# Kernel tuning notes

Measured on AMD Instinct MI355X. Metric: run time of the kernel, lower is better.

Reference implementation:

```python
import jax, jax.numpy as jnp
import numpy as np
from jax import lax

B = 2
IMG = 640.0
MIN_LEVEL, MAX_LEVEL = 3, 7
NUM_CLASSES = 91          # includes background (index 0)
MAX_TOTAL = 100
IOU_THR = 0.3
SCORE_THR = 0.05
PRE_NMS = 5000
BBOX_CLIP = float(np.log(1000.0 / 16.0))  # standard box-transform clip


def _level_anchors(level):
    """RetinaNet-style anchors for one pyramid level, [H*W*9, 4] in (y1,x1,y2,x2)."""
    stride = 2 ** level
    feat = int(IMG) // stride
    cy = (np.arange(feat, dtype=np.float32) + 0.5) * stride
    cx = (np.arange(feat, dtype=np.float32) + 0.5) * stride
    cy, cx = np.meshgrid(cy, cx, indexing='ij')
    base = 4.0 * stride
    anchors = []
    for octave in (2 ** 0.0, 2 ** (1.0 / 3.0), 2 ** (2.0 / 3.0)):
        for ar in (0.5, 1.0, 2.0):
            h = base * octave * np.sqrt(ar)
            w = base * octave / np.sqrt(ar)
            anchors.append(np.stack([cy - h / 2, cx - w / 2, cy + h / 2, cx + w / 2], -1))
    a = np.stack(anchors, -2).reshape(-1, 4)
    return a.astype(np.float32)


def setup_inputs():
    key = jax.random.key(0)
    inp = {}
    for level in range(MIN_LEVEL, MAX_LEVEL + 1):
        anc = _level_anchors(level)
        n = anc.shape[0]
        key, kb, kc = jax.random.split(key, 3)
        inp[f'box_outputs_{level}'] = 0.2 * jax.random.normal(kb, (B, n, 4), jnp.float32)
        inp[f'class_outputs_{level}'] = jax.random.normal(kc, (B, n, NUM_CLASSES), jnp.float32) - 2.0
        inp[f'anchor_boxes_{level}'] = jnp.broadcast_to(jnp.asarray(anc)[None], (B, n, 4))
    inp['image_shape'] = jnp.full((B, 2), IMG, jnp.float32)
    return inp


def _decode_boxes(enc, anchors):
    # faithful to box_utils.decode_boxes (with the +1/-1 pixel convention)
    dy, dx = enc[..., 0], enc[..., 1]
    dh = jnp.minimum(enc[..., 2], BBOX_CLIP)
    dw = jnp.minimum(enc[..., 3], BBOX_CLIP)
    ah = anchors[..., 2] - anchors[..., 0] + 1.0
    aw = anchors[..., 3] - anchors[..., 1] + 1.0
    ayc = anchors[..., 0] + 0.5 * ah
    axc = anchors[..., 1] + 0.5 * aw
    yc = dy * ah + ayc
    xc = dx * aw + axc
    h = jnp.exp(dh) * ah
    w = jnp.exp(dw) * aw
    ymin = yc - 0.5 * h
    xmin = xc - 0.5 * w
    return jnp.stack([ymin, xmin, ymin + h - 1.0, xmin + w - 1.0], axis=-1)


def _clip_boxes(boxes, image_shape):
    h = image_shape[:, 0:1]
    w = image_shape[:, 1:2]
    max_len = jnp.stack([h, w, h, w], axis=-1)  # [B,1,4]
    return jnp.clip(boxes, 0.0, max_len)


def _greedy_nms(scores, boxes):
    """Sorted greedy NMS over one (batch, class) lane.
    scores: [K] sorted descending (filtered entries are -1), boxes: [K,4].
    Returns top MAX_TOTAL selected (score, box) in descending score order,
    padded with score=-1 / zero boxes (matches sorted_non_max_suppression_padded).
    """
    areas = (boxes[:, 2] - boxes[:, 0]) * (boxes[:, 3] - boxes[:, 1])

    def step(active, _):
        masked = jnp.where(active, scores, -jnp.inf)
        i = jnp.argmax(masked)
        s = masked[i]
        valid = s > -1.0
        b = boxes[i]
        yy1 = jnp.maximum(b[0], boxes[:, 0])
        xx1 = jnp.maximum(b[1], boxes[:, 1])
        yy2 = jnp.minimum(b[2], boxes[:, 2])
        xx2 = jnp.minimum(b[3], boxes[:, 3])
        inter = jnp.maximum(yy2 - yy1, 0.0) * jnp.maximum(xx2 - xx1, 0.0)
        iou = inter / ((b[2] - b[0]) * (b[3] - b[1]) + areas - inter + 1e-8)
        active = active & (iou <= IOU_THR)
        active = active.at[i].set(False)
        out_s = jnp.where(valid, s, -1.0)
        out_b = jnp.where(valid, b, jnp.zeros_like(b))
        return active, (out_s, out_b)

    _, (sel_s, sel_b) = lax.scan(step, jnp.ones(scores.shape[0], bool), None, length=MAX_TOTAL)
    return sel_s, sel_b


def reference(box_outputs_3, box_outputs_4, box_outputs_5, box_outputs_6, box_outputs_7,
              class_outputs_3, class_outputs_4, class_outputs_5, class_outputs_6, class_outputs_7,
              anchor_boxes_3, anchor_boxes_4, anchor_boxes_5, anchor_boxes_6, anchor_boxes_7,
              image_shape):
    box_list = [box_outputs_3, box_outputs_4, box_outputs_5, box_outputs_6, box_outputs_7]
    cls_list = [class_outputs_3, class_outputs_4, class_outputs_5, class_outputs_6, class_outputs_7]
    anc_list = [anchor_boxes_3, anchor_boxes_4, anchor_boxes_5, anchor_boxes_6, anchor_boxes_7]

    boxes, scores = [], []
    for bo, co, an in zip(box_list, cls_list, anc_list):
        scores.append(jax.nn.sigmoid(co)[..., 1:])            # drop background class 0
        boxes.append(_clip_boxes(_decode_boxes(bo, an), image_shape))
    boxes = jnp.concatenate(boxes, axis=1)                     # [B,N,4] class-agnostic
    scores = jnp.concatenate(scores, axis=1)                   # [B,N,C]

    scores_t = jnp.transpose(scores, (0, 2, 1))                # [B,C,N]
    k = min(scores_t.shape[-1], PRE_NMS)
    top_s, idx = lax.top_k(scores_t, k)                        # [B,C,K]
    top_b = jax.vmap(lambda b, i: b[i])(boxes, idx)            # [B,C,K,4]

    # filter_boxes_by_scores: score -> -1, boxes -> 0 below threshold
    mask = top_s >= SCORE_THR
    top_s = jnp.where(mask, top_s, -1.0)
    top_b = top_b * mask[..., None].astype(top_b.dtype)

    sel_s, sel_b = jax.vmap(jax.vmap(_greedy_nms))(top_s, top_b)  # [B,C,T], [B,C,T,4]
    Bsz, C, T = sel_s.shape
    classes = jnp.broadcast_to(jnp.arange(C, dtype=jnp.int32)[None, :, None], (Bsz, C, T))

    flat_s = sel_s.reshape(Bsz, C * T)
    flat_b = sel_b.reshape(Bsz, C * T, 4)
    flat_c = classes.reshape(Bsz, C * T)

    final_s, fidx = lax.top_k(flat_s, MAX_TOTAL)
    final_b = jnp.take_along_axis(flat_b, fidx[..., None], axis=1)
    final_c = jnp.take_along_axis(flat_c, fidx, axis=1) + 1    # nmsed_classes += 1
    valid = jnp.sum((final_s > -1.0).astype(jnp.int32), axis=1)
    return final_b, final_s, final_c, valid
```

## Files before the change

### kernel.cpp

```cpp
#include <hip/hip_runtime.h>
#include <hip/hip_bf16.h>

typedef unsigned long long u64;
typedef unsigned int u32;

#define A_TOTAL 76725
#define NCLS 90
#define KTOP 5000u
#define MAXT 100
#define KTHR 0x3D4CCCCDu
#define TCAP 2048u
#define NSEL 384u

__device__ __forceinline__ u64 pack_key(u32 k, u32 i) {
  return ((u64)k << 32) | (u64)(0xFFFFFFFFu - i);
}

__device__ __forceinline__ int dig05(u64 k) {
  float s = __uint_as_float((u32)(k >> 32));
  int d = (int)((s - 0.5f) * 8175.0f);
  return min(max(d, 0), 4095);
}

__device__ __forceinline__ void cut4096w(const u32* hh, u32 need, int wl,
                                         u32& B, u32& incl, u32& above, u32& total) {
  int lo = wl << 6;
  u32 s = 0;
  #pragma unroll
  for (int j = 0; j < 64; ++j) s += hh[lo + j];
  u32 suf = s;
  #pragma unroll
  for (int off = 1; off < 64; off <<= 1) {
    u32 v = __shfl_down(suf, off, 64);
    if (wl < 64 - off) suf += v;
  }
  total = __shfl(suf, 0, 64);
  if (total < need) { B = 0; incl = total; above = 0; return; }
  u32 sufnext = suf - s;
  bool cross = (suf >= need) && (sufnext < need);
  u64 bal = __ballot(cross);
  int gl = (int)__ffsll((unsigned long long)bal) - 1;
  int glo = gl << 6;
  u32 aboveG = __shfl(sufnext, gl, 64);
  u32 hb = hh[glo + wl];
  u32 sufb = hb;
  #pragma unroll
  for (int off = 1; off < 64; off <<= 1) {
    u32 v = __shfl_down(sufb, off, 64);
    if (wl < 64 - off) sufb += v;
  }
  bool c2 = (aboveG + sufb >= need) && (aboveG + sufb - hb < need);
  u64 bal2 = __ballot(c2);
  int jB = (int)__ffsll((unsigned long long)bal2) - 1;
  B = (u32)(glo + jB);
  incl = aboveG + __shfl(sufb, jB, 64);
  above = incl - __shfl(hb, jB, 64);
}

__device__ __forceinline__ void bitonic_desc(u64* a, u32 n, int tid, int nth) {
  u32 P = 2; while (P < n) P <<= 1;
  for (u32 i = tid; i < P; i += nth) if (i >= n) a[i] = 0ULL;
  __syncthreads();
  for (u32 kk = 2; kk <= P; kk <<= 1) {
    for (u32 jj = kk >> 1; jj; jj >>= 1) {
      for (u32 i = tid; i < P; i += nth) {
        u32 ixj = i ^ jj;
        if (ixj > i) {
          u64 x = a[i], y = a[ixj];
          bool up = ((i & kk) == 0);
          if (up ? (x < y) : (x > y)) { a[i] = y; a[ixj] = x; }
        }
      }
      __syncthreads();
    }
  }
}

__device__ __forceinline__ int lazy_scan_g(const u64* key_s, const float4* boxes4, size_t bbase,
                                           int C, float4* wbox, float* outS, float* outB,
                                           int w, int wl, int* endCur) {
  int cur = 0;
  while (w < MAXT && cur < C) {
    int p = cur + wl;
    bool alive = (p < C);
    u64 kk = alive ? key_s[p] : 0ull;
    float4 mybox = make_float4(0.f, 0.f, 0.f, 0.f);
    if (alive) {
      u32 idx = 0xFFFFFFFFu - (u32)(kk & 0xFFFFFFFFull);
      mybox = boxes4[bbase + idx];
    }
    float myarea = alive ? (mybox.z - mybox.x) * (mybox.w - mybox.y) : 0.f;
    for (int j = 0; j < w; ++j) {
      if (alive) {
        float4 pb = wbox[j];
        float yy1 = fmaxf(pb.x, mybox.x), xx1 = fmaxf(pb.y, mybox.y);
        float yy2 = fminf(pb.z, mybox.z), xx2 = fminf(pb.w, mybox.w);
        float inter = fmaxf(yy2 - yy1, 0.0f) * fmaxf(xx2 - xx1, 0.0f);
        float pa = (pb.z - pb.x) * (pb.w - pb.y);
        if (inter / (pa + myarea - inter + 1e-8f) > 0.3f) alive = false;
      }
    }
    for (;;) {
      u64 bal = __ballot(alive);
      if (bal == 0ull) break;
      int js = (int)__ffsll((unsigned long long)bal) - 1;
      float4 pb;
      pb.x = __shfl(mybox.x, js, 64);
      pb.y = __shfl(mybox.y, js, 64);
      pb.z = __shfl(mybox.z, js, 64);
      pb.w = __shfl(mybox.w, js, 64);
      u64 wk = __shfl(kk, js, 64);
      if (wl == 0) {
        outS[w] = __uint_as_float((u32)(wk >> 32));
        *(float4*)(outB + w * 4) = pb;
        wbox[w] = pb;
      }
      w++;
      if (w >= MAXT) break;
      if (wl <= js) alive = false;
      else if (alive) {
        float yy1 = fmaxf(pb.x, mybox.x), xx1 = fmaxf(pb.y, mybox.y);
        float yy2 = fminf(pb.z, mybox.z), xx2 = fminf(pb.w, mybox.w);
        float inter = fmaxf(yy2 - yy1, 0.0f) * fmaxf(xx2 - xx1, 0.0f);
        float pa = (pb.z - pb.x) * (pb.w - pb.y);
        if (inter / (pa + myarea - inter + 1e-8f) > 0.3f) alive = false;
      }
    }
    cur += 64;
  }
  *endCur = cur;
  return w;
}

__device__ __forceinline__ void coll_elem(int i, float x, int b, int base,
                                          u64* __restrict__ listT_g, u32* __restrict__ cnt_pad) {
  if (x >= 0.0f) {
    u32 a = (u32)i / 91u;
    u32 c = (u32)i - a * 91u;
    if (c != 0u) {
      float s = 1.0f / (1.0f + expf(-x));
      int lane = b * NCLS + (int)c - 1;
      u32 idx = (u32)base + a;
      u32 p = atomicAdd(&cnt_pad[lane * 64], 1u);
      if (p < TCAP) listT_g[(size_t)lane * TCAP + p] = pack_key(__float_as_uint(s), idx);
    }
  }
}

__global__ __launch_bounds__(256) void front_kernel(
    const float* __restrict__ bx0, const float* __restrict__ bx1, const float* __restrict__ bx2,
    const float* __restrict__ bx3, const float* __restrict__ bx4,
    const float* __restrict__ an0, const float* __restrict__ an1, const float* __restrict__ an2,
    const float* __restrict__ an3, const float* __restrict__ an4,
    const float* __restrict__ c3, const float* __restrict__ c4, const float* __restrict__ c5,
    const float* __restrict__ c6, const float* __restrict__ c7,
    const float* __restrict__ img, float* __restrict__ boxes,
    u64* __restrict__ listT_g, u32* __restrict__ cnt_pad)
{
  int blk = blockIdx.x, tid = threadIdx.x;
  if (blk < 600) {
    int t = blk * 256 + tid;
    if (t >= 2 * A_TOTAL) return;
    int b = t / A_TOTAL, a = t % A_TOTAL;
    const float* bp; const float* ap; int al; int nl;
    if (a < 57600)      { bp = bx0; ap = an0; al = a;          nl = 57600; }
    else if (a < 72000) { bp = bx1; ap = an1; al = a - 57600;  nl = 14400; }
    else if (a < 75600) { bp = bx2; ap = an2; al = a - 72000;  nl = 3600;  }
    else if (a < 76500) { bp = bx3; ap = an3; al = a - 75600;  nl = 900;   }
    else                { bp = bx4; ap = an4; al = a - 76500;  nl = 225;   }
    float4 e  = *(const float4*)(bp + ((size_t)b * nl + al) * 4);
    float4 an = *(const float4*)(ap + ((size_t)b * nl + al) * 4);
    const float CLIP = 4.135166556742356f;
    float ah  = an.z - an.x + 1.0f;
    float aw  = an.w - an.y + 1.0f;
    float ayc = an.x + 0.5f * ah;
    float axc = an.y + 0.5f * aw;
    float dh = fminf(e.z, CLIP), dw = fminf(e.w, CLIP);
    float yc = e.x * ah + ayc;
    float xc = e.y * aw + axc;
    float h  = expf(dh) * ah;
    float w  = expf(dw) * aw;
    float ymin = yc - 0.5f * h;
    float xmin = xc - 0.5f * w;
    float ymax = ymin + h - 1.0f;
    float xmax = xmin + w - 1.0f;
    float H = img[b * 2 + 0], W = img[b * 2 + 1];
    float4 o;
    o.x = fminf(fmaxf(ymin, 0.0f), H);
    o.y = fminf(fmaxf(xmin, 0.0f), W);
    o.z = fminf(fmaxf(ymax, 0.0f), H);
    o.w = fminf(fmaxf(xmax, 0.0f), W);
    *(float4*)(boxes + (size_t)t * 4) = o;
    return;
  }
  int blk2 = blk - 600;
  const float* cls; int n, base, b, loc, J, lvl;
  if (blk2 < 1280)      { lvl = 0; cls = c3; n = 57600; base = 0;     J = 640; int r = blk2;        b = r >= J; loc = b ? r - J : r; }
  else if (blk2 < 1600) { lvl = 1; cls = c4; n = 14400; base = 57600; J = 160; int r = blk2 - 1280; b = r >= J; loc = b ? r - J : r; }
  else if (blk2 < 1680) { lvl = 2; cls = c5; n = 3600;  base = 72000; J = 40;  int r = blk2 - 1600; b = r >= J; loc = b ? r - J : r; }
  else if (blk2 < 1700) { lvl = 3; cls = c6; n = 900;   base = 75600; J = 10;  int r = blk2 - 1680; b = r >= J; loc = b ? r - J : r; }
  else                  { lvl = 4; cls = c7; n = 225;   base = 76500; J = 5;   int r = blk2 - 1700; b = r >= J; loc = b ? r - J : r; }

  if (lvl <= 3) {
    int F4 = n * 91 / 4;
    int chunk = (F4 + J - 1) / J;
    int q0 = loc * chunk;
    int q1 = q0 + chunk; if (q1 > F4) q1 = F4;
    const float4* src4 = (const float4*)(cls + (size_t)b * n * 91);
    for (int q = q0 + tid; q < q1; q += 256) {
      float4 v = src4[q];
      int i0 = q << 2;
      coll_elem(i0,     v.x, b, base, listT_g, cnt_pad);
      coll_elem(i0 + 1, v.y, b, base, listT_g, cnt_pad);
      coll_elem(i0 + 2, v.z, b, base, listT_g, cnt_pad);
      coll_elem(i0 + 3, v.w, b, base, listT_g, cnt_pad);
    }
  } else {
    int F = n * 91;
    int chunk = (F + J - 1) / J;
    int s0 = loc * chunk;
    int s1 = s0 + chunk; if (s1 > F) s1 = F;
    const float* src = cls + (size_t)b * F;
    for (int i = s0 + tid; i < s1; i += 256) coll_elem(i, src[i], b, base, listT_g, cnt_pad);
  }
}

__global__ __launch_bounds__(256) void nms_kernel(
    const float* __restrict__ c3, const float* __restrict__ c4, const float* __restrict__ c5,
    const float* __restrict__ c6, const float* __restrict__ c7,
    const float* __restrict__ boxes, const u64* __restrict__ listT_g,
    const u32* __restrict__ cnt_pad, float* __restrict__ nms_s, float* __restrict__ nms_b)
{
  __shared__ __align__(16) char big[40960];
  __shared__ __align__(16) u64 listE[2048];
  __shared__ u64 key_s[2048];
  __shared__ __align__(16) u32 histL[4096];
  __shared__ float4 wbox[MAXT];
  __shared__ u32 wtot[4];
  __shared__ u32 sh_flag, sh_mid, sh_bigS, sh_cS;
  __shared__ u64 sh_minPrev;
  __shared__ u32 sh_w, sh_done, sh_eidx, sh_Rthr, sh_eSorted, sh_bigF;
  __shared__ u32 sh_B, sh_incl, sh_above, sh_total, sh_cA, sh_cE, sh_B2;

  int tid = threadIdx.x;
  int lane = blockIdx.x;
  int b = lane / NCLS, c = lane % NCLS;
  const float4* boxes4 = (const float4*)boxes;
  size_t bbase = (size_t)b * A_TOTAL;
  const u64 thrpack = ((u64)KTHR) << 32;

  float* outS = nms_s + (size_t)lane * MAXT;
  float* outB = nms_b + (size_t)lane * MAXT * 4;

  u32 cnt = cnt_pad[lane * 64];
  if (tid == 0) { sh_flag = (cnt > TCAP) ? 1u : 0u; sh_mid = 0; sh_bigS = 0; }
  __syncthreads();

  if (!sh_flag) {
    const u64* LT = listT_g + (size_t)lane * TCAP;
    u64 kr[8];
    #pragma unroll
    for (int r = 0; r < 8; ++r) {
      u32 s = (u32)tid + (u32)r * 256u;
      kr[r] = (s < cnt) ? LT[s] : 0ull;
    }

    for (int i = tid; i < 4096; i += 256) histL[i] = 0;
    __syncthreads();
    #pragma unroll
    for (int r = 0; r < 8; ++r) if (kr[r]) atomicAdd(&histL[dig05(kr[r])], 1u);
    __syncthreads();
    if (tid < 64) {
      u32 Bx, ix, ax, tx;
      cut4096w(histL, NSEL, tid, Bx, ix, ax, tx);
      if (tid == 0) { sh_B = Bx; sh_incl = ix; sh_total = tx; sh_cS = 0; }
    }
    __syncthreads();
    u32 B = sh_B, incl = sh_incl, total = sh_total;
    bool selAll = (total < NSEL);
    u32 Csel = selAll ? total : incl;
    if (Csel <= 768u) {
      u64* sel = (u64*)histL;
      #pragma unroll
      for (int r = 0; r < 8; ++r) {
        u64 k = kr[r];
        if (k && (selAll || (u32)dig05(k) >= B)) {
          u32 p = atomicAdd(&sh_cS, 1u);
          if (p < 768u) sel[p] = k;
        }
      }
      __syncthreads();
      u32 Cs = sh_cS; if (Cs > 768u) Cs = 768u;
      for (u32 j = tid; j < Cs; j += 256) {
        u64 kj = sel[j];
        u32 rk = 0;
        for (u32 i2 = 0; i2 < Cs; ++i2) rk += (sel[i2] > kj) ? 1u : 0u;
        key_s[rk] = kj;
      }
      __syncthreads();
      if (tid < 64) {
        int ec;
        int w = lazy_scan_g(key_s, boxes4, bbase, (int)Cs, wbox, outS, outB, 0, tid, &ec);
        if (tid == 0) {
          sh_w = (u32)w;
          if (w < MAXT) { if (selAll) sh_flag = 1; else sh_mid = 1; }
          else if (!selAll && ec > (int)Cs - 64) sh_mid = 1;
        }
      }
    } else {
      if (tid == 0) sh_mid = 1;
    }
    __syncthreads();

    if (sh_mid && !sh_flag) {
      for (int i = tid; i < 4096; i += 256) histL[i] = 0;
      if (tid == 0) sh_bigS = 0;
      __syncthreads();
      #pragma unroll
      for (int r = 0; r < 8; ++r) if (kr[r]) atomicAdd(&histL[dig05(kr[r])], 1u);
      __syncthreads();
      {
        int t0 = tid << 4;
        u32 hloc[16]; u32 ssum = 0;
        #pragma unroll
        for (int j = 0; j < 16; ++j) { hloc[j] = histL[t0 + j]; ssum += hloc[j]; }
        int wl = tid & 63, wid = tid >> 6;
        u32 suf = ssum;
        #pragma unroll
        for (int off = 1; off < 64; off <<= 1) {
          u32 v = __shfl_down(suf, off, 64);
          if (wl < 64 - off) suf += v;
        }
        if (wl == 0) wtot[wid] = suf;
        __syncthreads();
        u32 cross = 0;
        for (int w2 = wid + 1; w2 < 4; ++w2) cross += wtot[w2];
        u32 run = (suf - ssum) + cross;
        #pragma unroll
        for (int j = 15; j >= 0; --j) { u32 b2 = run; run += hloc[j]; histL[t0 + j] = b2; }
      }
      __syncthreads();
      #pragma unroll
      for (int r = 0; r < 8; ++r) {
        u64 k = kr[r];
        if (k) {
          u32 pos = atomicAdd(&histL[dig05(k)], 1u);
          if (pos < TCAP) key_s[pos] = k;
        }
      }
      __syncthreads();
      {
        int t0 = tid << 4;
        for (int j = 0; j < 16; ++j) {
          u32 d = (u32)(t0 + j);
          u32 end = histL[d];
          u32 start = (d == 4095u) ? 0u : histL[d + 1];
          u32 cc = end - start;
          if (cc >= 2u) {
            if (cc <= 48u) {
              for (u32 a2 = start + 1; a2 < end; ++a2) {
                u64 kv = key_s[a2];
                int bi = (int)a2 - 1;
                while (bi >= (int)start && key_s[bi] < kv) { key_s[bi + 1] = key_s[bi]; --bi; }
                key_s[bi + 1] = kv;
              }
            } else sh_bigS = 1;
          }
        }
      }
      __syncthreads();
      if (sh_bigS) bitonic_desc(key_s, cnt, tid, 256);
      if (tid < 64) {
        int ec;
        int w = lazy_scan_g(key_s, boxes4, bbase, (int)cnt, wbox, outS, outB, 0, tid, &ec);
        if (tid == 0) {
          sh_w = (u32)w;
          if (w < MAXT) sh_flag = 1;
        }
      }
    }
  }
  __syncthreads();
  if (!sh_flag) {
    u32 w = sh_w;
    for (u32 p = w + (u32)tid; p < MAXT; p += 256) {
      outS[p] = -1.0f;
      *(float4*)(outB + p * 4) = make_float4(0.f, 0.f, 0.f, 0.f);
    }
    return;
  }

  auto sb_of = [&](int i) -> u32 {
    const float* p; int al, nl;
    if (i < 57600)      { p = c3; al = i;          nl = 57600; }
    else if (i < 72000) { p = c4; al = i - 57600;  nl = 14400; }
    else if (i < 75600) { p = c5; al = i - 72000;  nl = 3600;  }
    else if (i < 76500) { p = c6; al = i - 75600;  nl = 900;   }
    else                { p = c7; al = i - 76500;  nl = 225;   }
    float x = p[((size_t)b * nl + al) * 91 + (c + 1)];
    float s = 1.0f / (1.0f + expf(-x));
    return __float_as_uint(s);
  };

  u64* listA = (u64*)big;
  for (int i = tid; i < 4096; i += 256) histL[i] = 0;
  if (tid == 0) {
    sh_cA = 0; sh_cE = 0; sh_w = 0; sh_done = 0; sh_eidx = 0; sh_eSorted = 0; sh_minPrev = ~0ull;
  }
  __syncthreads();
  for (int i = tid; i < A_TOTAL; i += 256) atomicAdd(&histL[sb_of(i) >> 19], 1u);
  __syncthreads();
  if (tid < 64) {
    u32 Bx, ix, ax, tx;
    cut4096w(histL, KTOP, tid, Bx, ix, ax, tx);
    if (tid == 0) sh_B = Bx;
  }
  __syncthreads();
  u32 B = sh_B;
  for (int i = tid; i < A_TOTAL; i += 256) {
    u32 u = sb_of(i);
    u32 bkt = u >> 19;
    if (bkt > B) {
      u32 p = atomicAdd(&sh_cA, 1u);
      if (p < 5120u) listA[p] = pack_key(u, (u32)i);
    } else if (bkt == B) {
      u32 p = atomicAdd(&sh_cE, 1u);
      if (p < 2048u) listE[p] = pack_key(u, (u32)i);
    }
  }
  __syncthreads();
  u32 g = sh_cA, h = sh_cE;
  if (h > 2048u) {
    for (int i = tid; i < 4096; i += 256) histL[i] = 0;
    if (tid == 0) sh_cE = 0;
    __syncthreads();
    for (int i = tid; i < A_TOTAL; i += 256) {
      u32 u = sb_of(i);
      if ((u >> 19) == B) atomicAdd(&histL[(u >> 7) & 0xFFFu], 1u);
    }
    __syncthreads();
    u32 R1 = KTOP - g;
    if (tid < 64) {
      u32 Bx, ix, ax, tx;
      cut4096w(histL, R1, tid, Bx, ix, ax, tx);
      if (tid == 0) sh_B2 = Bx;
    }
    __syncthreads();
    u32 B2 = sh_B2;
    for (int i = tid; i < A_TOTAL; i += 256) {
      u32 u = sb_of(i);
      if ((u >> 19) == B) {
        u32 sb2 = (u >> 7) & 0xFFFu;
        if (sb2 > B2) {
          u32 p = atomicAdd(&sh_cA, 1u);
          if (p < 5120u) listA[p] = pack_key(u, (u32)i);
        } else if (sb2 == B2) {
          u32 p = atomicAdd(&sh_cE, 1u);
          if (p < 2048u) listE[p] = pack_key(u, (u32)i);
        }
      }
    }
    __syncthreads();
    g = sh_cA; h = sh_cE; if (h > 2048u) h = 2048u;
  }
  if (g > 5120u) g = 5120u;
  u32 R = (g < KTOP) ? (KTOP - g) : 0u; if (R > h) R = h;

  u64 ak[20];
  #pragma unroll
  for (int r = 0; r < 20; ++r) {
    u32 s2 = (u32)tid + (u32)r * 256u;
    u64 kp = (s2 < g) ? listA[s2] : 0ull;
    if (kp < thrpack) kp = 0ull;
    ak[r] = kp;
  }
  __syncthreads();
  u32* cntArr = (u32*)big;

  const float LO0  = 0.04f;
  const float INV0 = 4096.0f / (1.001f - 0.04f);

  for (int seg = 0; seg < 7200; ++seg) {
    __syncthreads();
    if (sh_w >= MAXT || sh_done) break;
    u64 minPrev = sh_minPrev;

    int digLvl = 0;
    u32 A_B0 = 0, A_B1 = 0;
    float lo1 = 0.f, inv1 = 0.f;
    u64 kMask = 0, kPref = 0;
    int m1shift = 32;
    int selMode = -1;
    u32 selB = 0;
    u32 C = 0;
    bool fromE = false;

    for (int lvl = 0; lvl < 8; ++lvl) {
      for (int i = tid; i < 4096; i += 256) histL[i] = 0;
      __syncthreads();
      #pragma unroll
      for (int r = 0; r < 20; ++r) {
        u64 k = ak[r];
        if (!k || k >= minPrev) continue;
        float s = __uint_as_float((u32)(k >> 32));
        if (digLvl >= 1) { int d0 = (int)((s - LO0) * INV0); d0 = min(max(d0, 0), 4095); if ((u32)d0 != A_B0) continue; }
        if (digLvl >= 2) { int d1 = (int)((s - lo1) * inv1); d1 = min(max(d1, 0), 4095); if ((u32)d1 != A_B1) continue; }
        if (digLvl >= 3 && ((k & kMask) != kPref)) continue;
        u32 d;
        if (digLvl == 0)      { int t0 = (int)((s - LO0) * INV0); d = (u32)min(max(t0, 0), 4095); }
        else if (digLvl == 1) { int t1 = (int)((s - lo1) * inv1); d = (u32)min(max(t1, 0), 4095); }
        else                  d = (u32)((k >> m1shift) & 0xFFFull);
        atomicAdd(&histL[d], 1u);
      }
      __syncthreads();
      if (tid < 64) {
        u32 Bx, ix, ax, tx;
        cut4096w(histL, 1024u, tid, Bx, ix, ax, tx);
        if (tid == 0) { sh_B = Bx; sh_incl = ix; sh_above = ax; sh_total = tx; }
      }
      __syncthreads();
      u32 total = sh_total, incl = sh_incl, above = sh_above, Bx = sh_B;
      if (total == 0u)   { fromE = true; break; }
      if (total < 1024u) { selMode = 0; C = total; break; }
      if (incl <= 2048u) { selMode = 1; selB = Bx; C = incl; break; }
      if (above > 0u)    { selMode = 2; selB = Bx; C = above; break; }
      if (digLvl == 0) {
        A_B0 = Bx;
        lo1 = LO0 + (float)Bx / INV0;
        inv1 = INV0 * 4096.0f;
        digLvl = 1;
      } else if (digLvl == 1) {
        A_B1 = Bx;
        digLvl = 2; m1shift = 32;
      } else {
        kPref |= ((u64)Bx << m1shift);
        kMask |= (0xFFFull << m1shift);
        m1shift -= 12;
        digLvl++;
      }
      __syncthreads();
    }

    if (fromE) {
      if (!sh_eSorted) {
        bitonic_desc(listE, h, tid, 256);
        if (tid == 0) {
          u32 lo = 0, hi2 = h;
          while (lo < hi2) { u32 mid = (lo + hi2) >> 1; if (listE[mid] >= thrpack) lo = mid + 1; else hi2 = mid; }
          sh_Rthr = (R < lo) ? R : lo;
          sh_eSorted = 1;
        }
        __syncthreads();
      }
      u32 eidx = sh_eidx;
      u32 take = (sh_Rthr > eidx) ? (sh_Rthr - eidx) : 0u;
      if (take > 2048u) take = 2048u;
      if (take == 0u) { if (tid == 0) sh_done = 1; continue; }
      for (u32 i = tid; i < take; i += 256) key_s[i] = listE[eidx + i];
      C = take;
      if (tid == 0) sh_eidx = eidx + take;
    } else {
      u32 hloc[16];
      {
        int t0 = tid << 4;
        u32 ssum = 0;
        #pragma unroll
        for (int j = 0; j < 16; ++j) { hloc[j] = histL[t0 + j]; ssum += hloc[j]; }
        int wl = tid & 63, wid = tid >> 6;
        u32 suf = ssum;
        #pragma unroll
        for (int off = 1; off < 64; off <<= 1) {
          u32 v = __shfl_down(suf, off, 64);
          if (wl < 64 - off) suf += v;
        }
        if (wl == 0) wtot[wid] = suf;
        __syncthreads();
        u32 cross = 0;
        for (int w2 = wid + 1; w2 < 4; ++w2) cross += wtot[w2];
        u32 run = (suf - ssum) + cross;
        #pragma unroll
        for (int j = 15; j >= 0; --j) { u32 base2 = run; run += hloc[j]; histL[t0 + j] = base2; }
      }
      for (int i = tid; i < 4096; i += 256) cntArr[i] = 0;
      if (tid == 0) sh_bigF = 0;
      __syncthreads();
      #pragma unroll
      for (int r = 0; r < 20; ++r) {
        u64 k = ak[r];
        if (!k || k >= minPrev) continue;
        float s = __uint_as_float((u32)(k >> 32));
        if (digLvl >= 1) { int d0 = (int)((s - LO0) * INV0); d0 = min(max(d0, 0), 4095); if ((u32)d0 != A_B0) continue; }
        if (digLvl >= 2) { int d1 = (int)((s - lo1) * inv1); d1 = min(max(d1, 0), 4095); if ((u32)d1 != A_B1) continue; }
        if (digLvl >= 3 && ((k & kMask) != kPref)) continue;
        u32 d;
        if (digLvl == 0)      { int t0x = (int)((s - LO0) * INV0); d = (u32)min(max(t0x, 0), 4095); }
        else if (digLvl == 1) { int t1x = (int)((s - lo1) * inv1); d = (u32)min(max(t1x, 0), 4095); }
        else                  d = (u32)((k >> m1shift) & 0xFFFull);
        if (selMode == 1)      { if (d < selB) continue; }
        else if (selMode == 2) { if (d <= selB) continue; }
        u32 pos = histL[d] + atomicAdd(&cntArr[d], 1u);
        if (pos < 2048u) key_s[pos] = k;
      }
      __syncthreads();
      {
        int t0 = tid << 4;
        for (int j = 0; j < 16; ++j) {
          u32 bkt = (u32)(t0 + j);
          u32 cc = cntArr[bkt];
          if (cc >= 2u) {
            if (cc <= 48u) {
              u32 basep = histL[bkt];
              for (u32 a2 = 1; a2 < cc; ++a2) {
                u64 kv = key_s[basep + a2];
                int bi = (int)a2 - 1;
                while (bi >= 0 && key_s[basep + bi] < kv) { key_s[basep + bi + 1] = key_s[basep + bi]; --bi; }
                key_s[basep + bi + 1] = kv;
              }
            } else sh_bigF = 1;
          }
        }
      }
      __syncthreads();
      if (sh_bigF) bitonic_desc(key_s, C, tid, 256);
      if (tid == 0) sh_minPrev = key_s[C - 1];
    }
    __syncthreads();

    if (tid < 64) {
      int ec;
      int w = lazy_scan_g(key_s, boxes4, bbase, (int)C, wbox, outS, outB, (int)sh_w, tid, &ec);
      if (tid == 0) sh_w = (u32)w;
    }
  }

  __syncthreads();
  u32 w = sh_w;
  for (u32 p = w + (u32)tid; p < MAXT; p += 256) {
    outS[p] = -1.0f;
    *(float4*)(outB + p * 4) = make_float4(0.f, 0.f, 0.f, 0.f);
  }
}

__global__ __launch_bounds__(256) void merge_kernel(
    const float* __restrict__ nms_s, const float* __restrict__ nms_b,
    float* __restrict__ out_b, float* __restrict__ out_s,
    float* __restrict__ out_c, float* __restrict__ out_v)
{
  __shared__ u64 keys[NCLS * MAXT];
  __shared__ u32 hist[4096];
  __shared__ u64 sel[640];
  __shared__ u32 sh_cnt, sh_valid;
  __shared__ u32 sh_B, sh_incl, sh_above, sh_total;

  int b = blockIdx.x, tid = threadIdx.x;
  const int NTOT = NCLS * MAXT;

  for (int i = tid; i < NTOT; i += 256) {
    float s = nms_s[(size_t)b * NTOT + i];
    u32 u = __float_as_uint(s);
    u = (u & 0x80000000u) ? ~u : (u | 0x80000000u);
    keys[i] = ((u64)u << 32) | (u64)(0xFFFFFFFFu - (u32)i);
  }
  if (tid == 0) { sh_cnt = 0; sh_valid = 0; }

  u64 prefVal = 0;
  u64 T = 0;
  u32 need = MAXT;
  const int shifts[6] = {52, 40, 28, 16, 4, 0};
  const int widths[6] = {12, 12, 12, 12, 12, 4};
  for (int lvl = 0; lvl < 6; ++lvl) {
    int s = shifts[lvl], w = widths[lvl];
    for (int i = tid; i < 4096; i += 256) hist[i] = 0;
    __syncthreads();
    u32 dmask = (1u << w) - 1u;
    for (int i = tid; i < NTOT; i += 256) {
      u64 k = keys[i];
      if (lvl > 0 && (k >> (s + w)) != (prefVal >> (s + w))) continue;
      atomicAdd(&hist[(u32)((k >> s) & dmask)], 1u);
    }
    __syncthreads();
    if (tid < 64) {
      u32 Bx, ix, ax, tx;
      cut4096w(hist, need, tid, Bx, ix, ax, tx);
      if (tid == 0) { sh_B = Bx; sh_incl = ix; sh_above = ax; sh_total = tx; }
    }
    __syncthreads();
    u32 B = sh_B, incl = sh_incl, above = sh_above;
    if (incl <= 512u || lvl == 5) {
      T = prefVal | ((u64)B << s);
      break;
    }
    prefVal |= ((u64)B << s);
    need -= above;
  }
  __syncthreads();

  for (int i = tid; i < NTOT; i += 256) {
    u64 k = keys[i];
    if (k >= T) {
      u32 p = atomicAdd(&sh_cnt, 1u);
      if (p < 640u) sel[p] = k;
    }
  }
  __syncthreads();
  u32 cnt = sh_cnt; if (cnt > 640u) cnt = 640u;

  for (u32 j = tid; j < cnt; j += 256) {
    u64 kj = sel[j];
    u32 r = 0;
    for (u32 i = 0; i < cnt; ++i) r += (sel[i] > kj) ? 1u : 0u;
    if (r < (u32)MAXT) {
      u32 u = (u32)(kj >> 32);
      u32 bits = (u & 0x80000000u) ? (u ^ 0x80000000u) : ~u;
      float sc = __uint_as_float(bits);
      u32 flat = 0xFFFFFFFFu - (u32)(kj & 0xFFFFFFFFull);
      int cls = (int)(flat / MAXT), pos = (int)(flat % MAXT);
      out_s[b * MAXT + r] = sc;
      out_c[b * MAXT + r] = (float)(cls + 1);
      *(float4*)(out_b + ((size_t)b * MAXT + r) * 4) =
          *(const float4*)(nms_b + (((size_t)b * NCLS + cls) * MAXT + pos) * 4);
      if (sc > -1.0f) atomicAdd(&sh_valid, 1u);
    }
  }
  __syncthreads();
  if (tid == 0) out_v[b] = (float)sh_valid;
}

extern "C" void kernel_launch(void* const* d_in, const int* in_sizes, int n_in,
                              void* d_out, int out_size, void* d_ws, size_t ws_size,
                              hipStream_t stream)
{
  const float* box[5]; const float* cls[5]; const float* anc[5];
  bool interleaved = (in_sizes[1] == 2 * 57600 * 91);
  if (interleaved) {
    for (int l = 0; l < 5; ++l) {
      box[l] = (const float*)d_in[3 * l + 0];
      cls[l] = (const float*)d_in[3 * l + 1];
      anc[l] = (const float*)d_in[3 * l + 2];
    }
  } else {
    for (int l = 0; l < 5; ++l) {
      box[l] = (const float*)d_in[l];
      cls[l] = (const float*)d_in[5 + l];
      anc[l] = (const float*)d_in[10 + l];
    }
  }
  const float* img = (const float*)d_in[15];

  float* ws = (float*)d_ws;
  float* boxes_ws = ws;
  u32*   cnt_pad  = (u32*)(boxes_ws + 613800);
  u64*   listT_g  = (u64*)(cnt_pad + 180 * 64);
  float* nms_s    = (float*)(listT_g + 180 * 2048);
  float* nms_b    = nms_s + 18000;

  hipMemsetAsync(cnt_pad, 0, 180 * 64 * sizeof(u32), stream);

  front_kernel<<<2310, 256, 0, stream>>>(
      box[0], box[1], box[2], box[3], box[4],
      anc[0], anc[1], anc[2], anc[3], anc[4],
      cls[0], cls[1], cls[2], cls[3], cls[4],
      img, boxes_ws, listT_g, cnt_pad);

  nms_kernel<<<180, 256, 0, stream>>>(cls[0], cls[1], cls[2], cls[3], cls[4],
                                      boxes_ws, listT_g, cnt_pad, nms_s, nms_b);

  float* out_b = (float*)d_out;
  float* out_s = out_b + 800;
  float* out_c = out_s + 200;
  float* out_v = out_c + 200;
  merge_kernel<<<2, 256, 0, stream>>>(nms_s, nms_b, out_b, out_s, out_c, out_v);
}
```

Before: 119.5 us.

## Shard per-class candidate counters into 8 slices and double front grid

Spreads the per-class atomic counters across 8 slices chosen by block index, giving each slice its own 512-entry list, so fewer blocks contend on the same counter. The NMS kernel then takes a prefix sum over the slice counts to gather keys. The front kernel's class-collection grid is doubled so each block gets a smaller chunk. The IoU check now skips the division when there is no overlap. It also drops the end-cursor heuristic that set the mid flag, which may change which fallback path runs, and a slice overflowing 512 now forces the slow path.

```diff
diff --git a/kernel.cpp b/kernel.cpp
--- a/kernel.cpp
+++ b/kernel.cpp
@@ -10,6 +10,7 @@
 #define MAXT 100
 #define KTHR 0x3D4CCCCDu
 #define TCAP 2048u
+#define SCAP 512u
 #define NSEL 384u
 
 __device__ __forceinline__ u64 pack_key(u32 k, u32 i) {
@@ -78,7 +79,7 @@
 
 __device__ __forceinline__ int lazy_scan_g(const u64* key_s, const float4* boxes4, size_t bbase,
                                            int C, float4* wbox, float* outS, float* outB,
-                                           int w, int wl, int* endCur) {
+                                           int w, int wl) {
   int cur = 0;
   while (w < MAXT && cur < C) {
     int p = cur + wl;
@@ -96,8 +97,10 @@
         float yy1 = fmaxf(pb.x, mybox.x), xx1 = fmaxf(pb.y, mybox.y);
         float yy2 = fminf(pb.z, mybox.z), xx2 = fminf(pb.w, mybox.w);
         float inter = fmaxf(yy2 - yy1, 0.0f) * fmaxf(xx2 - xx1, 0.0f);
-        float pa = (pb.z - pb.x) * (pb.w - pb.y);
-        if (inter / (pa + myarea - inter + 1e-8f) > 0.3f) alive = false;
+        if (inter > 0.0f) {
+          float pa = (pb.z - pb.x) * (pb.w - pb.y);
+          if (inter / (pa + myarea - inter + 1e-8f) > 0.3f) alive = false;
+        }
       }
     }
     for (;;) {
@@ -122,17 +125,18 @@
         float yy1 = fmaxf(pb.x, mybox.x), xx1 = fmaxf(pb.y, mybox.y);
         float yy2 = fminf(pb.z, mybox.z), xx2 = fminf(pb.w, mybox.w);
         float inter = fmaxf(yy2 - yy1, 0.0f) * fmaxf(xx2 - xx1, 0.0f);
-        float pa = (pb.z - pb.x) * (pb.w - pb.y);
-        if (inter / (pa + myarea - inter + 1e-8f) > 0.3f) alive = false;
+        if (inter > 0.0f) {
+          float pa = (pb.z - pb.x) * (pb.w - pb.y);
+          if (inter / (pa + myarea - inter + 1e-8f) > 0.3f) alive = false;
+        }
       }
     }
     cur += 64;
   }
-  *endCur = cur;
   return w;
 }
 
-__device__ __forceinline__ void coll_elem(int i, float x, int b, int base,
+__device__ __forceinline__ void coll_elem(int i, float x, int b, int base, int slice,
                                           u64* __restrict__ listT_g, u32* __restrict__ cnt_pad) {
   if (x >= 0.0f) {
     u32 a = (u32)i / 91u;
@@ -141,8 +145,8 @@
       float s = 1.0f / (1.0f + expf(-x));
       int lane = b * NCLS + (int)c - 1;
       u32 idx = (u32)base + a;
-      u32 p = atomicAdd(&cnt_pad[lane * 64], 1u);
-      if (p < TCAP) listT_g[(size_t)lane * TCAP + p] = pack_key(__float_as_uint(s), idx);
+      u32 p = atomicAdd(&cnt_pad[lane * 128 + slice * 16], 1u);
+      if (p < SCAP) listT_g[(((size_t)lane * 8 + slice) << 9) + p] = pack_key(__float_as_uint(s), idx);
     }
   }
 }
@@ -194,12 +198,13 @@
     return;
   }
   int blk2 = blk - 600;
+  int slice = blk2 & 7;
   const float* cls; int n, base, b, loc, J, lvl;
-  if (blk2 < 1280)      { lvl = 0; cls = c3; n = 57600; base = 0;     J = 640; int r = blk2;        b = r >= J; loc = b ? r - J : r; }
-  else if (blk2 < 1600) { lvl = 1; cls = c4; n = 14400; base = 57600; J = 160; int r = blk2 - 1280; b = r >= J; loc = b ? r - J : r; }
-  else if (blk2 < 1680) { lvl = 2; cls = c5; n = 3600;  base = 72000; J = 40;  int r = blk2 - 1600; b = r >= J; loc = b ? r - J : r; }
-  else if (blk2 < 1700) { lvl = 3; cls = c6; n = 900;   base = 75600; J = 10;  int r = blk2 - 1680; b = r >= J; loc = b ? r - J : r; }
-  else                  { lvl = 4; cls = c7; n = 225;   base = 76500; J = 5;   int r = blk2 - 1700; b = r >= J; loc = b ? r - J : r; }
+  if (blk2 < 2560)      { lvl = 0; cls = c3; n = 57600; base = 0;     J = 1280; int r = blk2;        b = r >= J; loc = b ? r - J : r; }
+  else if (blk2 < 3200) { lvl = 1; cls = c4; n = 14400; base = 57600; J = 320;  int r = blk2 - 2560; b = r >= J; loc = b ? r - J : r; }
+  else if (blk2 < 3360) { lvl = 2; cls = c5; n = 3600;  base = 72000; J = 80;   int r = blk2 - 3200; b = r >= J; loc = b ? r - J : r; }
+  else if (blk2 < 3400) { lvl = 3; cls = c6; n = 900;   base = 75600; J = 20;   int r = blk2 - 3360; b = r >= J; loc = b ? r - J : r; }
+  else                  { lvl = 4; cls = c7; n = 225;   base = 76500; J = 10;   int r = blk2 - 3400; b = r >= J; loc = b ? r - J : r; }
 
   if (lvl <= 3) {
     int F4 = n * 91 / 4;
@@ -210,10 +215,10 @@
     for (int q = q0 + tid; q < q1; q += 256) {
       float4 v = src4[q];
       int i0 = q << 2;
-      coll_elem(i0,     v.x, b, base, listT_g, cnt_pad);
-      coll_elem(i0 + 1, v.y, b, base, listT_g, cnt_pad);
-      coll_elem(i0 + 2, v.z, b, base, listT_g, cnt_pad);
-      coll_elem(i0 + 3, v.w, b, base, listT_g, cnt_pad);
+      coll_elem(i0,     v.x, b, base, slice, listT_g, cnt_pad);
+      coll_elem(i0 + 1, v.y, b, base, slice, listT_g, cnt_pad);
+      coll_elem(i0 + 2, v.z, b, base, slice, listT_g, cnt_pad);
+      coll_elem(i0 + 3, v.w, b, base, slice, listT_g, cnt_pad);
     }
   } else {
     int F = n * 91;
@@ -221,7 +226,7 @@
     int s0 = loc * chunk;
     int s1 = s0 + chunk; if (s1 > F) s1 = F;
     const float* src = cls + (size_t)b * F;
-    for (int i = s0 + tid; i < s1; i += 256) coll_elem(i, src[i], b, base, listT_g, cnt_pad);
+    for (int i = s0 + tid; i < s1; i += 256) coll_elem(i, src[i], b, base, slice, listT_g, cnt_pad);
   }
 }
 
@@ -252,17 +257,31 @@
   float* outS = nms_s + (size_t)lane * MAXT;
   float* outB = nms_b + (size_t)lane * MAXT * 4;
 
-  u32 cnt = cnt_pad[lane * 64];
-  if (tid == 0) { sh_flag = (cnt > TCAP) ? 1u : 0u; sh_mid = 0; sh_bigS = 0; }
+  u32 pre[9]; pre[0] = 0;
+  bool of = false;
+  #pragma unroll
+  for (int j = 0; j < 8; ++j) {
+    u32 cj = cnt_pad[lane * 128 + j * 16];
+    of |= (cj > SCAP);
+    pre[j + 1] = pre[j] + cj;
+  }
+  u32 cnt = pre[8];
+  if (tid == 0) { sh_flag = (of || cnt > TCAP) ? 1u : 0u; sh_mid = 0; sh_bigS = 0; }
   __syncthreads();
 
   if (!sh_flag) {
-    const u64* LT = listT_g + (size_t)lane * TCAP;
     u64 kr[8];
     #pragma unroll
     for (int r = 0; r < 8; ++r) {
       u32 s = (u32)tid + (u32)r * 256u;
-      kr[r] = (s < cnt) ? LT[s] : 0ull;
+      u64 k = 0ull;
+      if (s < cnt) {
+        u32 j = 0;
+        #pragma unroll
+        for (int t = 1; t < 8; ++t) if (s >= pre[t]) j = (u32)t;
+        k = listT_g[(((size_t)lane * 8 + j) << 9) + (s - pre[j])];
+      }
+      kr[r] = k;
     }
 
     for (int i = tid; i < 4096; i += 256) histL[i] = 0;
@@ -299,12 +318,10 @@
       }
       __syncthreads();
       if (tid < 64) {
-        int ec;
-        int w = lazy_scan_g(key_s, boxes4, bbase, (int)Cs, wbox, outS, outB, 0, tid, &ec);
+        int w = lazy_scan_g(key_s, boxes4, bbase, (int)Cs, wbox, outS, outB, 0, tid);
         if (tid == 0) {
           sh_w = (u32)w;
           if (w < MAXT) { if (selAll) sh_flag = 1; else sh_mid = 1; }
-          else if (!selAll && ec > (int)Cs - 64) sh_mid = 1;
         }
       }
     } else {
@@ -371,8 +388,7 @@
       __syncthreads();
       if (sh_bigS) bitonic_desc(key_s, cnt, tid, 256);
       if (tid < 64) {
-        int ec;
-        int w = lazy_scan_g(key_s, boxes4, bbase, (int)cnt, wbox, outS, outB, 0, tid, &ec);
+        int w = lazy_scan_g(key_s, boxes4, bbase, (int)cnt, wbox, outS, outB, 0, tid);
         if (tid == 0) {
           sh_w = (u32)w;
           if (w < MAXT) sh_flag = 1;
@@ -627,8 +643,7 @@
     __syncthreads();
 
     if (tid < 64) {
-      int ec;
-      int w = lazy_scan_g(key_s, boxes4, bbase, (int)C, wbox, outS, outB, (int)sh_w, tid, &ec);
+      int w = lazy_scan_g(key_s, boxes4, bbase, (int)C, wbox, outS, outB, (int)sh_w, tid);
       if (tid == 0) sh_w = (u32)w;
     }
   }
@@ -750,13 +765,13 @@
   float* ws = (float*)d_ws;
   float* boxes_ws = ws;
   u32*   cnt_pad  = (u32*)(boxes_ws + 613800);
-  u64*   listT_g  = (u64*)(cnt_pad + 180 * 64);
-  float* nms_s    = (float*)(listT_g + 180 * 2048);
+  u64*   listT_g  = (u64*)(cnt_pad + 180 * 128);
+  float* nms_s    = (float*)(listT_g + 180 * 8 * 512);
   float* nms_b    = nms_s + 18000;
 
-  hipMemsetAsync(cnt_pad, 0, 180 * 64 * sizeof(u32), stream);
-
-  front_kernel<<<2310, 256, 0, stream>>>(
+  hipMemsetAsync(cnt_pad, 0, 180 * 128 * sizeof(u32), stream);
+
+  front_kernel<<<4020, 256, 0, stream>>>(
       box[0], box[1], box[2], box[3], box[4],
       anc[0], anc[1], anc[2], anc[3], anc[4],
       cls[0], cls[1], cls[2], cls[3], cls[4],
```

Result: faster. 114.9 us (-3.8%).
